# Kernel optimization log

Hardware: AMD Instinct MI355X
Metric: run time of the kernel (lower is better)

## Reference

```python
import jax, jax.numpy as jnp
import numpy as np

K = 1024  # attention hidden dim
H = 1024  # encoder hidden dim


def setup_inputs() -> dict:
    key = jax.random.key(0)
    ks = jax.random.split(key, 8)
    B, S = 32, 2048
    decoder_state = jax.random.normal(ks[0], (B, H), dtype=jnp.float32)
    encoder_hiddens = jax.random.normal(ks[1], (B, S, H), dtype=jnp.float32)
    # Linear params (torch convention: y = x @ W.T + b)
    Wa_w = jax.random.normal(ks[2], (1, K), dtype=jnp.float32) / np.sqrt(K)
    Wa_b = jnp.zeros((1,), dtype=jnp.float32)
    Wb_w = jax.random.normal(ks[3], (K, H), dtype=jnp.float32) / np.sqrt(H)
    Wb_b = jnp.zeros((K,), dtype=jnp.float32)
    Wc_w = jax.random.normal(ks[4], (K, H), dtype=jnp.float32) / np.sqrt(H)
    Wc_b = jnp.zeros((K,), dtype=jnp.float32)
    return {
        "decoder_state": decoder_state,
        "encoder_hiddens": encoder_hiddens,
        "Wa_w": Wa_w, "Wa_b": Wa_b,
        "Wb_w": Wb_w, "Wb_b": Wb_b,
        "Wc_w": Wc_w, "Wc_b": Wc_b,
    }


def reference(decoder_state, encoder_hiddens, Wa_w, Wa_b, Wb_w, Wb_b, Wc_w, Wc_b):
    # dec_proj: [B, K]; enc_proj: [B, S, K]
    dec_proj = decoder_state @ Wb_w.T + Wb_b
    enc_proj = jnp.einsum('bsh,kh->bsk', encoder_hiddens, Wc_w) + Wc_b
    # additive score: tanh then project to scalar -> [B, S]
    e = jnp.tanh(dec_proj[:, None, :] + enc_proj)
    scores = jnp.einsum('bsk,k->bs', e, Wa_w[0]) + Wa_b[0]
    attn = jax.nn.softmax(scores, axis=1)
    # weighted sum over sequence -> [B, H]
    context = jnp.einsum('bs,bsh->bh', attn, encoder_hiddens)
    return context
```

## Files before the change

### kernel.cpp

```cpp
#include <hip/hip_runtime.h>
#include <hip/hip_bf16.h>
#include <stdint.h>

#define B_SZ 32
#define S_SZ 2048
#define H_SZ 1024
#define K_SZ 1024
#define M_SZ (B_SZ * S_SZ)

typedef __attribute__((ext_vector_type(8))) short bf16x8;
typedef __attribute__((ext_vector_type(4))) float f32x4;
typedef __attribute__((ext_vector_type(16))) float f32x16;


__device__ __forceinline__ short f2bf_rne(float f) {
    uint32_t u = __builtin_bit_cast(uint32_t, f);
    u += 0x7fffu + ((u >> 16) & 1u);
    return (short)(u >> 16);
}

__device__ __forceinline__ float bf2f(unsigned short u) {
    return __builtin_bit_cast(float, (uint32_t)u << 16);
}

__device__ __forceinline__ float fast_tanh(float x) {
    float ex = __expf(2.0f * x);
    return 1.0f - 2.0f / (ex + 1.0f);
}


__global__ void cvt_bf16_k(const float* __restrict__ in,
                           __hip_bfloat16* __restrict__ out, int n8) {
    int idx = blockIdx.x * blockDim.x + threadIdx.x;
    int stride = gridDim.x * blockDim.x;
    for (int i = idx; i < n8; i += stride) {
        const float4* p = (const float4*)in + (size_t)i * 2;
        float4 a = p[0], b = p[1];
        bf16x8 r;
        r[0] = f2bf_rne(a.x); r[1] = f2bf_rne(a.y);
        r[2] = f2bf_rne(a.z); r[3] = f2bf_rne(a.w);
        r[4] = f2bf_rne(b.x); r[5] = f2bf_rne(b.y);
        r[6] = f2bf_rne(b.z); r[7] = f2bf_rne(b.w);
        ((bf16x8*)out)[i] = r;
    }
}


__global__ __launch_bounds__(256) void prep_k(
    const float* __restrict__ Wc, __hip_bfloat16* __restrict__ wc_bf,
    const float* __restrict__ ds, const float* __restrict__ Wb,
    const float* __restrict__ Wb_b, const float* __restrict__ Wc_b,
    float* __restrict__ dp) {
    if (blockIdx.x < 512) {
        int i = blockIdx.x * 256 + threadIdx.x;
        const float4* p = (const float4*)Wc + (size_t)i * 2;
        float4 a = p[0], b = p[1];
        bf16x8 r;
        r[0] = f2bf_rne(a.x); r[1] = f2bf_rne(a.y);
        r[2] = f2bf_rne(a.z); r[3] = f2bf_rne(a.w);
        r[4] = f2bf_rne(b.x); r[5] = f2bf_rne(b.y);
        r[6] = f2bf_rne(b.z); r[7] = f2bf_rne(b.w);
        ((bf16x8*)wc_bf)[i] = r;
        return;
    }
    int g = (blockIdx.x - 512) * 4 + (threadIdx.x >> 6);
    int lane = threadIdx.x & 63;
    int b = g >> 10;
    int k = g & 1023;
    const float4* wrow = (const float4*)(Wb + (size_t)k * H_SZ);
    const float4* xrow = (const float4*)(ds + (size_t)b * H_SZ);
    float sum = 0.f;
#pragma unroll
    for (int it = 0; it < 4; it++) {
        float4 w = wrow[lane + it * 64];
        float4 x = xrow[lane + it * 64];
        sum += w.x * x.x + w.y * x.y + w.z * x.z + w.w * x.w;
    }
#pragma unroll
    for (int off = 1; off < 64; off <<= 1) sum += __shfl_xor(sum, off, 64);
    if (lane == 0) dp[g] = sum + Wb_b[k] + Wc_b[k];
}


__global__ __launch_bounds__(256) void gemm_scores32_k(
    const __hip_bfloat16* __restrict__ Ab, const __hip_bfloat16* __restrict__ Bw,
    const float* __restrict__ decp, const float* __restrict__ Wa,
    float* __restrict__ sp) {
    __shared__ __align__(16) unsigned char AsmRaw[2 * 128 * 32 * 2];
    __shared__ __align__(16) unsigned char BsmRaw[2 * 128 * 32 * 2];

    const int t = threadIdx.x;
    const int wave = t >> 6;
    const int lane = t & 63;
    const int wm = wave >> 1, wn = wave & 1;
    const int l31 = lane & 31;
    const int half = lane >> 5;

    const int id = blockIdx.x;
    const int colBlk = (id >> 3) & 7;
    const int rowBlk = ((id >> 6) << 3) | (id & 7);
    const int row0 = rowBlk * 128;
    const int col0 = colBlk * 128;
    const int b = row0 >> 11;

    f32x16 acc[2][2];
#pragma unroll
    for (int i = 0; i < 2; i++)
#pragma unroll
        for (int j = 0; j < 2; j++)
#pragma unroll
            for (int r = 0; r < 16; r++) acc[i][j][r] = 0.f;

    for (int k0 = 0; k0 < H_SZ; k0 += 64) {
#pragma unroll
        for (int p = 0; p < 2; p++)
#pragma unroll
            for (int inst = 0; inst < 2; inst++) {
                int slot = inst * 256 + t;
                int r = slot >> 2, c8 = slot & 3;
                const __hip_bfloat16* gA = Ab + (size_t)(row0 + r) * H_SZ + k0 + p * 32 + c8 * 8;
                __builtin_amdgcn_global_load_lds(
                    (const __attribute__((address_space(1))) void*)gA,
                    (__attribute__((address_space(3))) void*)(AsmRaw + p * 8192 + inst * 4096 + wave * 1024),
                    16, 0, 0);
                const __hip_bfloat16* gB = Bw + (size_t)(col0 + r) * H_SZ + k0 + p * 32 + c8 * 8;
                __builtin_amdgcn_global_load_lds(
                    (const __attribute__((address_space(1))) void*)gB,
                    (__attribute__((address_space(3))) void*)(BsmRaw + p * 8192 + inst * 4096 + wave * 1024),
                    16, 0, 0);
            }
        __syncthreads();

#pragma unroll
        for (int ks = 0; ks < 4; ks++) {
            const int pOff = (ks >> 1) * 8192;
            const int cOff = (ks & 1) * 32 + half * 16;
            bf16x8 a0 = *(const bf16x8*)(AsmRaw + pOff + (wm * 64 + l31) * 64 + cOff);
            bf16x8 a1 = *(const bf16x8*)(AsmRaw + pOff + (wm * 64 + 32 + l31) * 64 + cOff);
            bf16x8 b0 = *(const bf16x8*)(BsmRaw + pOff + (wn * 64 + l31) * 64 + cOff);
            bf16x8 b1 = *(const bf16x8*)(BsmRaw + pOff + (wn * 64 + 32 + l31) * 64 + cOff);
            acc[0][0] = __builtin_amdgcn_mfma_f32_32x32x16_bf16(a0, b0, acc[0][0], 0, 0, 0);
            acc[0][1] = __builtin_amdgcn_mfma_f32_32x32x16_bf16(a0, b1, acc[0][1], 0, 0, 0);
            acc[1][0] = __builtin_amdgcn_mfma_f32_32x32x16_bf16(a1, b0, acc[1][0], 0, 0, 0);
            acc[1][1] = __builtin_amdgcn_mfma_f32_32x32x16_bf16(a1, b1, acc[1][1], 0, 0, 0);
        }
        __syncthreads();
    }

    float wa_j[2], dp_j[2];
#pragma unroll
    for (int j = 0; j < 2; j++) {
        int c = col0 + wn * 64 + j * 32 + l31;
        wa_j[j] = Wa[c];
        dp_j[j] = decp[b * K_SZ + c];
    }
    const int slotIdx = colBlk * 2 + wn;
#pragma unroll
    for (int i = 0; i < 2; i++) {
#pragma unroll
        for (int r = 0; r < 16; r++) {
            float v = wa_j[0] * fast_tanh(acc[i][0][r] + dp_j[0])
                    + wa_j[1] * fast_tanh(acc[i][1][r] + dp_j[1]);
#pragma unroll
            for (int off = 1; off < 32; off <<= 1) v += __shfl_xor(v, off, 64);
            if (l31 == 0) {
                int m = row0 + wm * 64 + i * 32 + (r & 3) + 8 * (r >> 2) + 4 * half;
                sp[(size_t)slotIdx * M_SZ + m] = v;
            }
        }
    }
}


__global__ __launch_bounds__(256) void gemm_scores_f32_k(
    const float* __restrict__ Af, const __hip_bfloat16* __restrict__ Bw,
    const float* __restrict__ decp, const float* __restrict__ Wa,
    float* __restrict__ sp) {
    __shared__ __align__(16) unsigned char AsmRaw[128 * 32 * 4];
    __shared__ __align__(16) unsigned char BsmRaw[128 * 32 * 2];
    const int t = threadIdx.x;
    const int wave = t >> 6;
    const int lane = t & 63;
    const int wm = wave >> 1, wn = wave & 1;
    const int quad = lane >> 4;
    const int l15 = lane & 15;
    const int id = blockIdx.x;
    const int colBlk = (id >> 3) & 7;
    const int rowBlk = ((id >> 6) << 3) | (id & 7);
    const int row0 = rowBlk * 128;
    const int col0 = colBlk * 128;
    const int b = row0 >> 11;
    f32x4 acc[4][4];
#pragma unroll
    for (int i = 0; i < 4; i++)
#pragma unroll
        for (int j = 0; j < 4; j++) acc[i][j] = f32x4{0.f, 0.f, 0.f, 0.f};
    for (int k0 = 0; k0 < H_SZ; k0 += 32) {
#pragma unroll
        for (int inst = 0; inst < 4; inst++) {
            int slot = inst * 256 + t;
            int r = slot >> 3, c4 = slot & 7;
            const float* g = Af + (size_t)(row0 + r) * H_SZ + k0 + c4 * 4;
            __builtin_amdgcn_global_load_lds(
                (const __attribute__((address_space(1))) void*)g,
                (__attribute__((address_space(3))) void*)(AsmRaw + inst * 4096 + wave * 1024),
                16, 0, 0);
        }
#pragma unroll
        for (int inst = 0; inst < 2; inst++) {
            int slot = inst * 256 + t;
            int r = slot >> 2, c8 = slot & 3;
            const __hip_bfloat16* g = Bw + (size_t)(col0 + r) * H_SZ + k0 + c8 * 8;
            __builtin_amdgcn_global_load_lds(
                (const __attribute__((address_space(1))) void*)g,
                (__attribute__((address_space(3))) void*)(BsmRaw + inst * 4096 + wave * 1024),
                16, 0, 0);
        }
        __syncthreads();
        bf16x8 afr[4], bfr[4];
#pragma unroll
        for (int i = 0; i < 4; i++) {
            int r = wm * 64 + i * 16 + l15;
            const float* ap = (const float*)AsmRaw + r * 32 + quad * 8;
            f32x4 lo = *(const f32x4*)ap;
            f32x4 hi = *(const f32x4*)(ap + 4);
            bf16x8 v;
            v[0] = f2bf_rne(lo[0]); v[1] = f2bf_rne(lo[1]);
            v[2] = f2bf_rne(lo[2]); v[3] = f2bf_rne(lo[3]);
            v[4] = f2bf_rne(hi[0]); v[5] = f2bf_rne(hi[1]);
            v[6] = f2bf_rne(hi[2]); v[7] = f2bf_rne(hi[3]);
            afr[i] = v;
        }
#pragma unroll
        for (int j = 0; j < 4; j++) {
            int r = wn * 64 + j * 16 + l15;
            bfr[j] = *(const bf16x8*)((const __hip_bfloat16*)BsmRaw + r * 32 + quad * 8);
        }
#pragma unroll
        for (int i = 0; i < 4; i++)
#pragma unroll
            for (int j = 0; j < 4; j++)
                acc[i][j] = __builtin_amdgcn_mfma_f32_16x16x32_bf16(afr[i], bfr[j], acc[i][j], 0, 0, 0);
        __syncthreads();
    }
    float wa_j[4], dp_j[4];
#pragma unroll
    for (int j = 0; j < 4; j++) {
        int c = col0 + wn * 64 + j * 16 + l15;
        wa_j[j] = Wa[c];
        dp_j[j] = decp[b * K_SZ + c];
    }
    const int slotIdx = colBlk * 2 + wn;
#pragma unroll
    for (int i = 0; i < 4; i++) {
#pragma unroll
        for (int r = 0; r < 4; r++) {
            float tsum = 0.f;
#pragma unroll
            for (int j = 0; j < 4; j++)
                tsum += wa_j[j] * fast_tanh(acc[i][j][r] + dp_j[j]);
#pragma unroll
            for (int off = 1; off < 16; off <<= 1) tsum += __shfl_xor(tsum, off, 64);
            if (l15 == 0) {
                int m = row0 + wm * 64 + i * 16 + quad * 4 + r;
                sp[(size_t)slotIdx * M_SZ + m] = tsum;
            }
        }
    }
}


__global__ __launch_bounds__(1024) void softmax_k(
    const float* __restrict__ sp, float* __restrict__ attn) {
    int b = blockIdx.x;
    int t = threadIdx.x;
    __shared__ float wred[16];
    __shared__ float wred2[16];
    float sc[2];
    float mx = -1e30f;
#pragma unroll
    for (int u = 0; u < 2; u++) {
        int m = b * S_SZ + t + u * 1024;
        float v = 0.f;
#pragma unroll
        for (int c = 0; c < 16; c++) v += sp[(size_t)c * M_SZ + m];
        sc[u] = v;
        mx = fmaxf(mx, v);
    }
#pragma unroll
    for (int off = 1; off < 64; off <<= 1) mx = fmaxf(mx, __shfl_xor(mx, off, 64));
    if ((t & 63) == 0) wred[t >> 6] = mx;
    __syncthreads();
#pragma unroll
    for (int w = 0; w < 16; w++) mx = fmaxf(mx, wred[w]);
    float lsum = 0.f;
#pragma unroll
    for (int u = 0; u < 2; u++) { sc[u] = expf(sc[u] - mx); lsum += sc[u]; }
#pragma unroll
    for (int off = 1; off < 64; off <<= 1) lsum += __shfl_xor(lsum, off, 64);
    if ((t & 63) == 0) wred2[t >> 6] = lsum;
    __syncthreads();
    float tot = 0.f;
#pragma unroll
    for (int w = 0; w < 16; w++) tot += wred2[w];
    float inv = 1.f / tot;
#pragma unroll
    for (int u = 0; u < 2; u++) attn[b * S_SZ + t + u * 1024] = sc[u] * inv;
}


template <bool BF16E>
__global__ __launch_bounds__(256) void ctx_part_k(
    const float* __restrict__ attn, const void* __restrict__ encp,
    float* __restrict__ cp) {
    int b = blockIdx.x >> 5;
    int c = blockIdx.x & 31;
    int t = threadIdx.x;
    __shared__ float wloc[64];
    if (t < 64) wloc[t] = attn[b * S_SZ + c * 64 + t];
    __syncthreads();
    float4 acc = {0.f, 0.f, 0.f, 0.f};
    if constexpr (BF16E) {
        const ushort4* ep = (const ushort4*)((const __hip_bfloat16*)encp +
                              ((size_t)b * S_SZ + (size_t)c * 64) * H_SZ);
#pragma unroll 8
        for (int s = 0; s < 64; s++) {
            float w = wloc[s];
            ushort4 v = ep[s * 256 + t];
            acc.x += w * bf2f(v.x); acc.y += w * bf2f(v.y);
            acc.z += w * bf2f(v.z); acc.w += w * bf2f(v.w);
        }
    } else {
        const float4* ep = (const float4*)((const float*)encp +
                              ((size_t)b * S_SZ + (size_t)c * 64) * H_SZ);
#pragma unroll 8
        for (int s = 0; s < 64; s++) {
            float w = wloc[s];
            float4 v = ep[s * 256 + t];
            acc.x += w * v.x; acc.y += w * v.y;
            acc.z += w * v.z; acc.w += w * v.w;
        }
    }
    ((float4*)(cp + ((size_t)c * B_SZ + b) * H_SZ))[t] = acc;
}

__global__ void ctx_red_k(const float* __restrict__ cp, float* __restrict__ out) {
    int i = blockIdx.x * blockDim.x + threadIdx.x;
    float s = 0.f;
#pragma unroll
    for (int c = 0; c < 32; c++) s += cp[(size_t)c * (B_SZ * H_SZ) + i];
    out[i] = s;
}


extern "C" void kernel_launch(void* const* d_in, const int* in_sizes, int n_in,
                              void* d_out, int out_size, void* d_ws, size_t ws_size,
                              hipStream_t stream) {
    const float* dec  = (const float*)d_in[0];
    const float* enc  = (const float*)d_in[1];
    const float* Wa_w = (const float*)d_in[2];
    const float* Wb_w = (const float*)d_in[4];
    const float* Wb_b = (const float*)d_in[5];
    const float* Wc_w = (const float*)d_in[6];
    const float* Wc_b = (const float*)d_in[7];
    float* out = (float*)d_out;

    char* ws = (char*)d_ws;
    size_t off = 0;
    auto alloc = [&](size_t bytes) -> void* {
        void* p = ws + off;
        off += (bytes + 255) & ~(size_t)255;
        return p;
    };
    __hip_bfloat16* wc_bf = (__hip_bfloat16*)alloc((size_t)K_SZ * H_SZ * 2);
    float* dp     = (float*)alloc((size_t)B_SZ * K_SZ * 4);
    float* spart  = (float*)alloc((size_t)16 * M_SZ * 4);
    float* attn   = (float*)alloc((size_t)B_SZ * S_SZ * 4);
    float* cpart  = (float*)alloc((size_t)32 * B_SZ * H_SZ * 4);
    __hip_bfloat16* enc_bf = (__hip_bfloat16*)alloc((size_t)M_SZ * H_SZ * 2);
    const bool useBf16A = (off <= ws_size);

    prep_k<<<512 + 8192, 256, 0, stream>>>(Wc_w, wc_bf, dec, Wb_w, Wb_b, Wc_b, dp);
    if (useBf16A) {
        cvt_bf16_k<<<8192, 256, 0, stream>>>(enc, enc_bf, M_SZ * H_SZ / 8);
        gemm_scores32_k<<<(M_SZ / 128) * 8, 256, 0, stream>>>(enc_bf, wc_bf, dp, Wa_w, spart);
    } else {
        gemm_scores_f32_k<<<(M_SZ / 128) * 8, 256, 0, stream>>>(enc, wc_bf, dp, Wa_w, spart);
    }
    softmax_k<<<B_SZ, 1024, 0, stream>>>(spart, attn);
    if (useBf16A)
        ctx_part_k<true><<<B_SZ * 32, 256, 0, stream>>>(attn, enc_bf, cpart);
    else
        ctx_part_k<false><<<B_SZ * 32, 256, 0, stream>>>(attn, enc, cpart);
    ctx_red_k<<<128, 256, 0, stream>>>(cpart, out);
}
```

Baseline: 649.0 us.

## Merge prep and convert kernels, register-stream A in GEMM, widen ctx loads

Folds the encoder bf16 conversion into the prep kernel so one launch does all three prep jobs. Rewrites the scores GEMM to use 16x16x32 MFMAs, with A fragments loaded straight from global memory into registers and prefetched one step ahead. Only B is staged through LDS, which cuts LDS use and allows an occupancy hint of 3. The context partial kernel now uses 8-wide bf16 loads, splits the sequence into two stripes and combines them through shared memory. The risks are uncoalesced direct A loads with no reuse across waves, which raises global traffic, and shorter k-steps with more barriers.

```diff
diff --git a/kernel.cpp b/kernel.cpp
--- a/kernel.cpp
+++ b/kernel.cpp
@@ -10,7 +10,6 @@
 
 typedef __attribute__((ext_vector_type(8))) short bf16x8;
 typedef __attribute__((ext_vector_type(4))) float f32x4;
-typedef __attribute__((ext_vector_type(16))) float f32x16;
 
 
 __device__ __forceinline__ short f2bf_rne(float f) {
@@ -29,28 +28,12 @@
 }
 
 
-__global__ void cvt_bf16_k(const float* __restrict__ in,
-                           __hip_bfloat16* __restrict__ out, int n8) {
-    int idx = blockIdx.x * blockDim.x + threadIdx.x;
-    int stride = gridDim.x * blockDim.x;
-    for (int i = idx; i < n8; i += stride) {
-        const float4* p = (const float4*)in + (size_t)i * 2;
-        float4 a = p[0], b = p[1];
-        bf16x8 r;
-        r[0] = f2bf_rne(a.x); r[1] = f2bf_rne(a.y);
-        r[2] = f2bf_rne(a.z); r[3] = f2bf_rne(a.w);
-        r[4] = f2bf_rne(b.x); r[5] = f2bf_rne(b.y);
-        r[6] = f2bf_rne(b.z); r[7] = f2bf_rne(b.w);
-        ((bf16x8*)out)[i] = r;
-    }
-}
-
-
-__global__ __launch_bounds__(256) void prep_k(
+__global__ __launch_bounds__(256) void prep_all_k(
     const float* __restrict__ Wc, __hip_bfloat16* __restrict__ wc_bf,
     const float* __restrict__ ds, const float* __restrict__ Wb,
     const float* __restrict__ Wb_b, const float* __restrict__ Wc_b,
-    float* __restrict__ dp) {
+    float* __restrict__ dp,
+    const float* __restrict__ enc, __hip_bfloat16* __restrict__ enc_bf) {
     if (blockIdx.x < 512) {
         int i = blockIdx.x * 256 + threadIdx.x;
         const float4* p = (const float4*)Wc + (size_t)i * 2;
@@ -63,38 +46,54 @@
         ((bf16x8*)wc_bf)[i] = r;
         return;
     }
-    int g = (blockIdx.x - 512) * 4 + (threadIdx.x >> 6);
-    int lane = threadIdx.x & 63;
-    int b = g >> 10;
-    int k = g & 1023;
-    const float4* wrow = (const float4*)(Wb + (size_t)k * H_SZ);
-    const float4* xrow = (const float4*)(ds + (size_t)b * H_SZ);
-    float sum = 0.f;
-#pragma unroll
-    for (int it = 0; it < 4; it++) {
-        float4 w = wrow[lane + it * 64];
-        float4 x = xrow[lane + it * 64];
-        sum += w.x * x.x + w.y * x.y + w.z * x.z + w.w * x.w;
-    }
-#pragma unroll
-    for (int off = 1; off < 64; off <<= 1) sum += __shfl_xor(sum, off, 64);
-    if (lane == 0) dp[g] = sum + Wb_b[k] + Wc_b[k];
-}
-
-
-__global__ __launch_bounds__(256) void gemm_scores32_k(
+    if (blockIdx.x < 8704) {
+        int g = (blockIdx.x - 512) * 4 + (threadIdx.x >> 6);
+        int lane = threadIdx.x & 63;
+        int b = g >> 10;
+        int k = g & 1023;
+        const float4* wrow = (const float4*)(Wb + (size_t)k * H_SZ);
+        const float4* xrow = (const float4*)(ds + (size_t)b * H_SZ);
+        float sum = 0.f;
+#pragma unroll
+        for (int it = 0; it < 4; it++) {
+            float4 w = wrow[lane + it * 64];
+            float4 x = xrow[lane + it * 64];
+            sum += w.x * x.x + w.y * x.y + w.z * x.z + w.w * x.w;
+        }
+#pragma unroll
+        for (int off = 1; off < 64; off <<= 1) sum += __shfl_xor(sum, off, 64);
+        if (lane == 0) dp[g] = sum + Wb_b[k] + Wc_b[k];
+        return;
+    }
+    int idx = (blockIdx.x - 8704) * 256 + threadIdx.x;
+    const int stride = 8192 * 256;
+#pragma unroll
+    for (int u = 0; u < 4; u++) {
+        int i = idx + u * stride;
+        const float4* p = (const float4*)enc + (size_t)i * 2;
+        float4 a = p[0], b = p[1];
+        bf16x8 r;
+        r[0] = f2bf_rne(a.x); r[1] = f2bf_rne(a.y);
+        r[2] = f2bf_rne(a.z); r[3] = f2bf_rne(a.w);
+        r[4] = f2bf_rne(b.x); r[5] = f2bf_rne(b.y);
+        r[6] = f2bf_rne(b.z); r[7] = f2bf_rne(b.w);
+        ((bf16x8*)enc_bf)[i] = r;
+    }
+}
+
+
+__global__ __launch_bounds__(256, 3) void gemm_scoresA_k(
     const __hip_bfloat16* __restrict__ Ab, const __hip_bfloat16* __restrict__ Bw,
     const float* __restrict__ decp, const float* __restrict__ Wa,
     float* __restrict__ sp) {
-    __shared__ __align__(16) unsigned char AsmRaw[2 * 128 * 32 * 2];
-    __shared__ __align__(16) unsigned char BsmRaw[2 * 128 * 32 * 2];
+    __shared__ __align__(16) unsigned char BsmRaw[128 * 32 * 2];
 
     const int t = threadIdx.x;
     const int wave = t >> 6;
     const int lane = t & 63;
     const int wm = wave >> 1, wn = wave & 1;
-    const int l31 = lane & 31;
-    const int half = lane >> 5;
+    const int quad = lane >> 4;
+    const int l15 = lane & 15;
 
     const int id = blockIdx.x;
     const int colBlk = (id >> 3) & 7;
@@ -103,69 +102,73 @@
     const int col0 = colBlk * 128;
     const int b = row0 >> 11;
 
-    f32x16 acc[2][2];
-#pragma unroll
-    for (int i = 0; i < 2; i++)
-#pragma unroll
-        for (int j = 0; j < 2; j++)
-#pragma unroll
-            for (int r = 0; r < 16; r++) acc[i][j][r] = 0.f;
-
-    for (int k0 = 0; k0 < H_SZ; k0 += 64) {
-#pragma unroll
-        for (int p = 0; p < 2; p++)
-#pragma unroll
-            for (int inst = 0; inst < 2; inst++) {
-                int slot = inst * 256 + t;
-                int r = slot >> 2, c8 = slot & 3;
-                const __hip_bfloat16* gA = Ab + (size_t)(row0 + r) * H_SZ + k0 + p * 32 + c8 * 8;
-                __builtin_amdgcn_global_load_lds(
-                    (const __attribute__((address_space(1))) void*)gA,
-                    (__attribute__((address_space(3))) void*)(AsmRaw + p * 8192 + inst * 4096 + wave * 1024),
-                    16, 0, 0);
-                const __hip_bfloat16* gB = Bw + (size_t)(col0 + r) * H_SZ + k0 + p * 32 + c8 * 8;
-                __builtin_amdgcn_global_load_lds(
-                    (const __attribute__((address_space(1))) void*)gB,
-                    (__attribute__((address_space(3))) void*)(BsmRaw + p * 8192 + inst * 4096 + wave * 1024),
-                    16, 0, 0);
-            }
-        __syncthreads();
-
-#pragma unroll
-        for (int ks = 0; ks < 4; ks++) {
-            const int pOff = (ks >> 1) * 8192;
-            const int cOff = (ks & 1) * 32 + half * 16;
-            bf16x8 a0 = *(const bf16x8*)(AsmRaw + pOff + (wm * 64 + l31) * 64 + cOff);
-            bf16x8 a1 = *(const bf16x8*)(AsmRaw + pOff + (wm * 64 + 32 + l31) * 64 + cOff);
-            bf16x8 b0 = *(const bf16x8*)(BsmRaw + pOff + (wn * 64 + l31) * 64 + cOff);
-            bf16x8 b1 = *(const bf16x8*)(BsmRaw + pOff + (wn * 64 + 32 + l31) * 64 + cOff);
-            acc[0][0] = __builtin_amdgcn_mfma_f32_32x32x16_bf16(a0, b0, acc[0][0], 0, 0, 0);
-            acc[0][1] = __builtin_amdgcn_mfma_f32_32x32x16_bf16(a0, b1, acc[0][1], 0, 0, 0);
-            acc[1][0] = __builtin_amdgcn_mfma_f32_32x32x16_bf16(a1, b0, acc[1][0], 0, 0, 0);
-            acc[1][1] = __builtin_amdgcn_mfma_f32_32x32x16_bf16(a1, b1, acc[1][1], 0, 0, 0);
-        }
-        __syncthreads();
-    }
-
-    float wa_j[2], dp_j[2];
-#pragma unroll
-    for (int j = 0; j < 2; j++) {
-        int c = col0 + wn * 64 + j * 32 + l31;
+    f32x4 acc[4][4];
+#pragma unroll
+    for (int i = 0; i < 4; i++)
+#pragma unroll
+        for (int j = 0; j < 4; j++) acc[i][j] = f32x4{0.f, 0.f, 0.f, 0.f};
+
+    const __hip_bfloat16* aBase = Ab + (size_t)(row0 + wm * 64 + l15) * H_SZ + quad * 8;
+    bf16x8 aCur[4], aNext[4];
+#pragma unroll
+    for (int i = 0; i < 4; i++)
+        aNext[i] = *(const bf16x8*)(aBase + (size_t)i * 16 * H_SZ);
+
+    for (int k0 = 0; k0 < H_SZ; k0 += 32) {
+#pragma unroll
+        for (int inst = 0; inst < 2; inst++) {
+            int slot = inst * 256 + t;
+            int r = slot >> 2, c8 = slot & 3;
+            const __hip_bfloat16* g = Bw + (size_t)(col0 + r) * H_SZ + k0 + c8 * 8;
+            __builtin_amdgcn_global_load_lds(
+                (const __attribute__((address_space(1))) void*)g,
+                (__attribute__((address_space(3))) void*)(BsmRaw + inst * 4096 + wave * 1024),
+                16, 0, 0);
+        }
+#pragma unroll
+        for (int i = 0; i < 4; i++) aCur[i] = aNext[i];
+        if (k0 + 32 < H_SZ) {
+#pragma unroll
+            for (int i = 0; i < 4; i++)
+                aNext[i] = *(const bf16x8*)(aBase + (size_t)i * 16 * H_SZ + k0 + 32);
+        }
+        __syncthreads();
+
+        bf16x8 bfr[4];
+#pragma unroll
+        for (int j = 0; j < 4; j++) {
+            int r = wn * 64 + j * 16 + l15;
+            bfr[j] = *(const bf16x8*)((const __hip_bfloat16*)BsmRaw + r * 32 + quad * 8);
+        }
+#pragma unroll
+        for (int i = 0; i < 4; i++)
+#pragma unroll
+            for (int j = 0; j < 4; j++)
+                acc[i][j] = __builtin_amdgcn_mfma_f32_16x16x32_bf16(aCur[i], bfr[j], acc[i][j], 0, 0, 0);
+        __syncthreads();
+    }
+
+    float wa_j[4], dp_j[4];
+#pragma unroll
+    for (int j = 0; j < 4; j++) {
+        int c = col0 + wn * 64 + j * 16 + l15;
         wa_j[j] = Wa[c];
         dp_j[j] = decp[b * K_SZ + c];
     }
     const int slotIdx = colBlk * 2 + wn;
 #pragma unroll
-    for (int i = 0; i < 2; i++) {
-#pragma unroll
-        for (int r = 0; r < 16; r++) {
-            float v = wa_j[0] * fast_tanh(acc[i][0][r] + dp_j[0])
-                    + wa_j[1] * fast_tanh(acc[i][1][r] + dp_j[1]);
-#pragma unroll
-            for (int off = 1; off < 32; off <<= 1) v += __shfl_xor(v, off, 64);
-            if (l31 == 0) {
-                int m = row0 + wm * 64 + i * 32 + (r & 3) + 8 * (r >> 2) + 4 * half;
-                sp[(size_t)slotIdx * M_SZ + m] = v;
+    for (int i = 0; i < 4; i++) {
+#pragma unroll
+        for (int r = 0; r < 4; r++) {
+            float tsum = 0.f;
+#pragma unroll
+            for (int j = 0; j < 4; j++)
+                tsum += wa_j[j] * fast_tanh(acc[i][j][r] + dp_j[j]);
+#pragma unroll
+            for (int off = 1; off < 16; off <<= 1) tsum += __shfl_xor(tsum, off, 64);
+            if (l15 == 0) {
+                int m = row0 + wm * 64 + i * 16 + quad * 4 + r;
+                sp[(size_t)slotIdx * M_SZ + m] = tsum;
             }
         }
     }
@@ -318,21 +321,41 @@
     int t = threadIdx.x;
     __shared__ float wloc[64];
     if (t < 64) wloc[t] = attn[b * S_SZ + c * 64 + t];
-    __syncthreads();
-    float4 acc = {0.f, 0.f, 0.f, 0.f};
     if constexpr (BF16E) {
-        const ushort4* ep = (const ushort4*)((const __hip_bfloat16*)encp +
-                              ((size_t)b * S_SZ + (size_t)c * 64) * H_SZ);
+        __shared__ float partial[128 * 8];
+        int oct = t & 127, stripe = t >> 7;
+        __syncthreads();
+        const __hip_bfloat16* ep = (const __hip_bfloat16*)encp +
+                                   ((size_t)b * S_SZ + (size_t)c * 64) * H_SZ;
+        float a[8] = {0.f, 0.f, 0.f, 0.f, 0.f, 0.f, 0.f, 0.f};
+        int s0 = stripe * 32;
 #pragma unroll 8
-        for (int s = 0; s < 64; s++) {
+        for (int s = s0; s < s0 + 32; s++) {
+            bf16x8 v = *(const bf16x8*)(ep + (size_t)s * H_SZ + oct * 8);
             float w = wloc[s];
-            ushort4 v = ep[s * 256 + t];
-            acc.x += w * bf2f(v.x); acc.y += w * bf2f(v.y);
-            acc.z += w * bf2f(v.z); acc.w += w * bf2f(v.w);
+#pragma unroll
+            for (int e = 0; e < 8; e++) a[e] += w * bf2f((unsigned short)v[e]);
+        }
+        if (stripe == 1) {
+#pragma unroll
+            for (int e = 0; e < 8; e++) partial[oct * 8 + e] = a[e];
+        }
+        __syncthreads();
+        if (stripe == 0) {
+            float* cpb = cp + ((size_t)c * B_SZ + b) * H_SZ + oct * 8;
+            float4 lo, hi;
+            lo.x = a[0] + partial[oct * 8 + 0]; lo.y = a[1] + partial[oct * 8 + 1];
+            lo.z = a[2] + partial[oct * 8 + 2]; lo.w = a[3] + partial[oct * 8 + 3];
+            hi.x = a[4] + partial[oct * 8 + 4]; hi.y = a[5] + partial[oct * 8 + 5];
+            hi.z = a[6] + partial[oct * 8 + 6]; hi.w = a[7] + partial[oct * 8 + 7];
+            *(float4*)cpb = lo;
+            *(float4*)(cpb + 4) = hi;
         }
     } else {
+        __syncthreads();
         const float4* ep = (const float4*)((const float*)encp +
                               ((size_t)b * S_SZ + (size_t)c * 64) * H_SZ);
+        float4 acc = {0.f, 0.f, 0.f, 0.f};
 #pragma unroll 8
         for (int s = 0; s < 64; s++) {
             float w = wloc[s];
@@ -340,8 +363,8 @@
             acc.x += w * v.x; acc.y += w * v.y;
             acc.z += w * v.z; acc.w += w * v.w;
         }
-    }
-    ((float4*)(cp + ((size_t)c * B_SZ + b) * H_SZ))[t] = acc;
+        ((float4*)(cp + ((size_t)c * B_SZ + b) * H_SZ))[t] = acc;
+    }
 }
 
 __global__ void ctx_red_k(const float* __restrict__ cp, float* __restrict__ out) {
@@ -380,13 +403,12 @@
     __hip_bfloat16* enc_bf = (__hip_bfloat16*)alloc((size_t)M_SZ * H_SZ * 2);
     const bool useBf16A = (off <= ws_size);
 
-    prep_k<<<512 + 8192, 256, 0, stream>>>(Wc_w, wc_bf, dec, Wb_w, Wb_b, Wc_b, dp);
-    if (useBf16A) {
-        cvt_bf16_k<<<8192, 256, 0, stream>>>(enc, enc_bf, M_SZ * H_SZ / 8);
-        gemm_scores32_k<<<(M_SZ / 128) * 8, 256, 0, stream>>>(enc_bf, wc_bf, dp, Wa_w, spart);
-    } else {
+    prep_all_k<<<useBf16A ? 16896 : 8704, 256, 0, stream>>>(
+        Wc_w, wc_bf, dec, Wb_w, Wb_b, Wc_b, dp, enc, enc_bf);
+    if (useBf16A)
+        gemm_scoresA_k<<<(M_SZ / 128) * 8, 256, 0, stream>>>(enc_bf, wc_bf, dp, Wa_w, spart);
+    else
         gemm_scores_f32_k<<<(M_SZ / 128) * 8, 256, 0, stream>>>(enc, wc_bf, dp, Wa_w, spart);
-    }
     softmax_k<<<B_SZ, 1024, 0, stream>>>(spart, attn);
     if (useBf16A)
         ctx_part_k<true><<<B_SZ * 32, 256, 0, stream>>>(attn, enc_bf, cpart);
```

New measurement: 719.0 us. +10.8%, slower.
